# Kernel optimization log

Measured on AMD Instinct MI355X. Metric: run time of the kernel, lower is better.

## Reference

```python
import jax, jax.numpy as jnp
import numpy as np

B, S, D = 16, 1024, 1024
H = 8
QK = D // 8            # qk_dim = dim / qk_dim_div(8) = 128
EXP = D * 2            # expand_dim = dim * expand_factor(2) = 2048
V = D                  # v_dim = dim
RESIDUAL_DEPTH = 384   # hyp['net']['residual_depth'] (init scale only)
NUM_BLOCKS = 8         # hyp['net']['num_blocks'] (init scale only)
NEG = -1e30            # stand-in for -inf in the masked positions


def setup_inputs() -> dict:
    key = jax.random.key(0)
    k0, k1, k2 = jax.random.split(key, 3)
    x = jax.random.normal(k0, (B, S, D), jnp.float32)
    norm_w = jnp.ones((D,), jnp.float32)  # LayerNorm weight (bias=False)
    expand_w = (0.5 / RESIDUAL_DEPTH**0.5 / 2.0) * jax.random.normal(
        k1, (2 * QK + 2 * EXP, D), jnp.float32)
    project_w = (1.0 / RESIDUAL_DEPTH**0.5 / 2.0 / NUM_BLOCKS) * jax.random.normal(
        k2, (D, EXP), jnp.float32)
    pos_bias_mult = jnp.array(1.0, jnp.float32)
    return {
        "x": x,
        "norm_w": norm_w,
        "expand_w": expand_w,
        "project_w": project_w,
        "pos_bias_mult": pos_bias_mult,
        "first_acting_token_idx": 512,
        "last_acting_token_idx": 768,
    }


def _make_mask(pos_bias_mult, seq_len, first_idx, last_idx, dtype):
    idx = jnp.arange(seq_len)
    rel = (idx[None, :] - idx[:, None]).astype(dtype)   # j - i  (ALiBi-like)
    causal = idx[None, :] <= idx[:, None]               # tril incl. diagonal
    bias = jax.nn.softplus(pos_bias_mult) * rel
    mask = jnp.where(causal, bias, NEG)
    if first_idx is not None:
        assert last_idx is not None and last_idx > first_idx
        # torch: idx >= seq_len -> None -> slice from 0
        fi = 0 if first_idx >= seq_len else first_idx
        li = 0 if last_idx >= seq_len else last_idx
        override = (idx[:, None] >= fi) & (idx[None, :] >= li)
        mask = jnp.where(override, bias, mask)
    return mask


def reference(x, norm_w, expand_w, project_w, pos_bias_mult,
              first_acting_token_idx, last_acting_token_idx):
    Bx, Sx, Dx = x.shape
    residual = x
    mask = _make_mask(pos_bias_mult, Sx, first_acting_token_idx,
                      last_acting_token_idx, x.dtype)  # [S, S]

    # LayerNorm (bias-free)
    mu = x.mean(-1, keepdims=True)
    xc = x - mu
    var = (xc * xc).mean(-1, keepdims=True)
    xn = xc * jax.lax.rsqrt(var + 1e-5) * norm_w

    # fused expand projection, then split q / k / linear / pre_gelu
    proj = jnp.einsum('bsd,ed->bse', xn, expand_w)
    q = proj[..., :QK]
    k = proj[..., QK:2 * QK]
    lin = proj[..., 2 * QK:2 * QK + EXP]
    pre = proj[..., 2 * QK + EXP:]
    geglu = lin * jax.nn.gelu(pre, approximate=False)

    # linear_value = False: both local and attention-value come from geglu
    geglu_local = geglu[..., :EXP - V]   # [B, S, EXP-V]
    geglu_value = geglu[..., EXP - V:]   # [B, S, V]

    dh_q = QK // H
    dh_v = V // H
    qh = q.reshape(Bx, Sx, H, dh_q).transpose(0, 2, 1, 3)
    kh = k.reshape(Bx, Sx, H, dh_q).transpose(0, 2, 1, 3)
    vh = geglu_value.reshape(Bx, Sx, H, dh_v).transpose(0, 2, 1, 3)

    scale = 1.0 / np.sqrt(dh_q)  # SDPA default: 1/sqrt(E), E = query head dim
    scores = jnp.einsum('bhqd,bhkd->bhqk', qh, kh) * scale + mask
    attn = jax.nn.softmax(scores, axis=-1)
    outh = jnp.einsum('bhqk,bhkd->bhqd', attn, vh)
    attention = outh.transpose(0, 2, 1, 3).reshape(Bx, Sx, V)
    # NOTE: geglu_local's head rearrange + inverse rearrange is an identity.

    out = jnp.einsum('bse,de->bsd',
                     jnp.concatenate([geglu_local, attention], axis=-1),
                     project_w)
    return residual + out
```

## Files before the change

### kernel.cpp

```cpp
#include <hip/hip_runtime.h>
#include <hip/hip_bf16.h>
#include <cstdint>
#include <cstddef>

#define S_LEN   1024
#define D_DIM   1024
#define QK_DIM  128
#define EXP_DIM 2048
#define H_HEADS 8
#define DH_Q    16
#define DH_V    128
#define M_ROWS  16384

typedef __bf16 bf16;
typedef __bf16 b16x4 __attribute__((ext_vector_type(4)));
typedef __bf16 b16x8 __attribute__((ext_vector_type(8)));
typedef float  fx4   __attribute__((ext_vector_type(4)));
typedef float  f32x16 __attribute__((ext_vector_type(16)));

__device__ __forceinline__ void load_lds16(const bf16* g, bf16* l) {
    __builtin_amdgcn_global_load_lds(
        (const __attribute__((address_space(1))) void*)g,
        (__attribute__((address_space(3))) void*)l, 16, 0, 0);
}

__global__ __launch_bounds__(256) void convert_kernel(const float* __restrict__ src,
                                                      bf16* __restrict__ dst, int n4) {
    const int i = blockIdx.x * 256 + threadIdx.x;
    if (i >= n4) return;
    const fx4 v = ((const fx4*)src)[i];
    b16x4 o;
#pragma unroll
    for (int k = 0; k < 4; ++k) o[k] = (bf16)v[k];
    ((b16x4*)dst)[i] = o;
}

__global__ __launch_bounds__(256) void convert_expand_kernel(const float* __restrict__ src,
                                                             bf16* __restrict__ dst) {
    const int i = blockIdx.x * 256 + threadIdx.x;
    const int orow = i >> 8, col = i & 255;
    int irow;
    if (orow < 256) {
        irow = orow;
    } else {
        const int t = orow - 256;
        const int c = t >> 5, j = t & 31;
        irow = (j < 16) ? (256 + c * 16 + j) : (2304 + c * 16 + (j - 16));
    }
    const fx4 v = ((const fx4*)src)[irow * 256 + col];
    b16x4 o;
#pragma unroll
    for (int k = 0; k < 4; ++k) o[k] = (bf16)v[k];
    ((b16x4*)dst)[i] = o;
}

__global__ __launch_bounds__(256) void ln_kernel(const float* __restrict__ x,
                                                 const float* __restrict__ w,
                                                 bf16* __restrict__ xn) {
    const int row = blockIdx.x;
    const int tid = threadIdx.x;
    const fx4 t = ((const fx4*)x)[(size_t)row * 256 + tid];
    float v[4];
    float s = 0.f, ss = 0.f;
#pragma unroll
    for (int i = 0; i < 4; ++i) { v[i] = t[i]; s += v[i]; ss += v[i] * v[i]; }
#pragma unroll
    for (int off = 32; off >= 1; off >>= 1) {
        s  += __shfl_xor(s,  off);
        ss += __shfl_xor(ss, off);
    }
    __shared__ float ls[4], lss[4];
    const int wave = tid >> 6;
    if ((tid & 63) == 0) { ls[wave] = s; lss[wave] = ss; }
    __syncthreads();
    s  = ls[0]  + ls[1]  + ls[2]  + ls[3];
    ss = lss[0] + lss[1] + lss[2] + lss[3];
    const float mu  = s * (1.f / D_DIM);
    const float var = ss * (1.f / D_DIM) - mu * mu;
    const float r   = rsqrtf(var + 1e-5f);
    const fx4 w4 = ((const fx4*)w)[tid];
    b16x4 o4;
#pragma unroll
    for (int i = 0; i < 4; ++i) o4[i] = (bf16)((v[i] - mu) * r * w4[i]);
    ((b16x4*)(xn + (size_t)row * D_DIM))[tid] = o4;
}

__device__ __forceinline__ float gelu_exact(float x) {
    return 0.5f * x * (1.f + erff(x * 0.70710678118654752f));
}

__device__ __forceinline__ void tile_map(int& tm, int& tn) {
    const int NT = gridDim.x, MT = gridDim.y;
    const int lin = blockIdx.y * NT + blockIdx.x;
    if ((MT & 31) == 0 && (NT & 3) == 0) {
        const int xcd = lin & 7, slot = lin >> 3;
        const int MB  = MT >> 3;
        const int cnc = NT >> 2;
        const int c = slot >> 4, w = slot & 15;
        const int cm = c / cnc, cn = c - cm * cnc;
        tm = xcd * MB + cm * 4 + (w >> 2);
        tn = cn * 4 + (w & 3);
    } else { tm = blockIdx.y; tn = blockIdx.x; }
}

template <int EPI>
__global__ __launch_bounds__(256) void gemm_bt(const bf16* __restrict__ A,
                                               const bf16* __restrict__ W,
                                               const float* __restrict__ R,
                                               bf16* __restrict__ C,
                                               bf16* __restrict__ VH,
                                               float* __restrict__ OutF,
                                               int M, int N, int K) {
    __shared__ bf16 As[128 * 32];
    __shared__ bf16 Ws[128 * 32];
    const int tid  = threadIdx.x;
    const int wave = tid >> 6, lane = tid & 63;
    int tmi, tni;
    tile_map(tmi, tni);
    const int tile_n = tni * 128;
    const int tile_m = tmi * 128;
    const int m_off = (wave >> 1) * 64, n_off = (wave & 1) * 64;

    fx4 acc[4][4] = {};

    const int c0 = wave * 128 + lane;
    const int c1 = c0 + 64;
    const int r0 = c0 >> 2, cc0 = (c0 & 3) * 8;
    const int r1 = c1 >> 2, cc1 = (c1 & 3) * 8;

    const int mrow = lane & 15, quad = lane >> 4;

    for (int k0 = 0; k0 < K; k0 += 32) {
        load_lds16(A + (size_t)(tile_m + r0) * K + k0 + cc0, &As[c0 * 8]);
        load_lds16(A + (size_t)(tile_m + r1) * K + k0 + cc1, &As[c1 * 8]);
        load_lds16(W + (size_t)(tile_n + r0) * K + k0 + cc0, &Ws[c0 * 8]);
        load_lds16(W + (size_t)(tile_n + r1) * K + k0 + cc1, &Ws[c1 * 8]);
        __syncthreads();

        b16x8 af[4], bfr[4];
#pragma unroll
        for (int i = 0; i < 4; ++i) {
            af[i]  = *(const b16x8*)&As[(m_off + i * 16 + mrow) * 32 + quad * 8];
            bfr[i] = *(const b16x8*)&Ws[(n_off + i * 16 + mrow) * 32 + quad * 8];
        }
#pragma unroll
        for (int mi = 0; mi < 4; ++mi)
#pragma unroll
            for (int ni = 0; ni < 4; ++ni)
                acc[mi][ni] = __builtin_amdgcn_mfma_f32_16x16x32_bf16(
                    af[mi], bfr[ni], acc[mi][ni], 0, 0, 0);
        __syncthreads();
    }

    const int lcol = lane & 15, lrow4 = (lane >> 4) * 4;
    if (EPI == 2) {
        const int gbase = ((tile_n + n_off) >> 1) + lcol;
#pragma unroll
        for (int mi = 0; mi < 4; ++mi)
#pragma unroll
            for (int np = 0; np < 2; ++np) {
                const int gcol = gbase + np * 16;
#pragma unroll
                for (int r = 0; r < 4; ++r) {
                    const int gr = tile_m + m_off + mi * 16 + lrow4 + r;
                    const float l = acc[mi][2 * np][r];
                    const float p = acc[mi][2 * np + 1][r];
                    const float g = l * gelu_exact(p);
                    if (gcol < 1024) C[(size_t)gr * 2048 + gcol] = (bf16)g;
                    else             VH[(size_t)gr * 1024 + (gcol - 1024)] = (bf16)g;
                }
            }
    } else {
#pragma unroll
        for (int mi = 0; mi < 4; ++mi)
#pragma unroll
            for (int ni = 0; ni < 4; ++ni)
#pragma unroll
                for (int r = 0; r < 4; ++r) {
                    const int gr = tile_m + m_off + mi * 16 + lrow4 + r;
                    const int gc = tile_n + n_off + ni * 16 + lcol;
                    const float a = acc[mi][ni][r];
                    if (EPI == 0) {
                        C[(size_t)gr * N + gc] = (bf16)a;
                    } else {
                        const size_t idx = (size_t)gr * N + gc;
                        OutF[idx] = a + R[idx];
                    }
                }
    }
}

__global__ __launch_bounds__(512) void attn_kernel(const bf16* __restrict__ qk,
                                                   const bf16* __restrict__ vh,
                                                   const float* __restrict__ pbmv,
                                                   const int* __restrict__ fip,
                                                   const int* __restrict__ lip,
                                                   bf16* __restrict__ concatb) {
    const int lin = blockIdx.y * gridDim.x + blockIdx.x;
    const int xcd = lin & 7, slot = lin >> 3;
    const int bh = xcd * 16 + (slot >> 3);
    const int qt = slot & 7;
    const int b = bh >> 3, h = bh & 7;
    const int q0 = qt * 128;
    const int tid  = threadIdx.x;
    const int wave = tid >> 6, lane = tid & 63;
    const int lm = lane & 31, lh = lane >> 5;
    const int qq = wave >> 1, sect = wave & 1;

    __shared__ float Ps[128][68];
    __shared__ bf16  Pb[128][72];
    __shared__ bf16  Vt[128][72];
    __shared__ float Mrow[128], Lrow[128], Arow[128];

    const float pm = pbmv[0];
    const float sp = (pm > 20.f) ? pm : log1pf(expf(pm));
    int fi = fip[0], li = lip[0];
    if (fi >= S_LEN) fi = 0;
    if (li >= S_LEN) li = 0;

    const b16x8 qfrag = *(const b16x8*)(qk
        + ((size_t)(b * S_LEN + q0 + qq * 32 + lm)) * 256 + h * DH_Q + lh * 8);

    f32x16 accO[2] = {};
    if (tid < 128) { Mrow[tid] = -3e38f; Lrow[tid] = 0.f; }

    const int vkey = tid & 63;
    const int vd   = (tid >> 6) * 16;
    const int srow = wave * 16 + (lane >> 2);
    const int skq  = (lane & 3) * 16;

    const int qmax = q0 + 127;
    for (int k0 = 0; k0 < S_LEN; k0 += 64) {
        const bool any = (k0 <= qmax) || ((qmax >= fi) && (k0 + 63 >= li));
        if (!any) continue;

        __syncthreads();

#pragma unroll
        for (int i = 0; i < 2; ++i) {
            const int d0 = vd + i * 8;
            const b16x8 v8 = *(const b16x8*)(vh
                + ((size_t)(b * S_LEN + k0 + vkey)) * D_DIM + h * DH_V + d0);
#pragma unroll
            for (int j = 0; j < 8; ++j) Vt[d0 + j][vkey] = v8[j];
        }

        {
            const b16x8 kfrag = *(const b16x8*)(qk
                + ((size_t)(b * S_LEN + k0 + sect * 32 + lm)) * 256
                + QK_DIM + h * DH_Q + lh * 8);
            f32x16 z = {};
            const f32x16 S = __builtin_amdgcn_mfma_f32_32x32x16_bf16(qfrag, kfrag, z, 0, 0, 0);
#pragma unroll
            for (int r = 0; r < 16; ++r) {
                const int row = qq * 32 + (r & 3) + 8 * (r >> 2) + 4 * lh;
                Ps[row][sect * 32 + lm] = S[r];
            }
        }
        __syncthreads();

        {
            const int rg = q0 + srow;
            float s[16];
#pragma unroll
            for (int i = 0; i < 4; ++i) {
                const fx4 t = *(const fx4*)&Ps[srow][skq + i * 4];
#pragma unroll
                for (int j = 0; j < 4; ++j) {
                    const int jg = k0 + skq + i * 4 + j;
                    const bool act = (jg <= rg) || ((rg >= fi) && (jg >= li));
                    s[i * 4 + j] = act ? (t[j] * 0.25f + sp * (float)(jg - rg)) : -3e38f;
                }
            }
            float mloc = -3e38f;
#pragma unroll
            for (int i = 0; i < 16; ++i) mloc = fmaxf(mloc, s[i]);
            mloc = fmaxf(mloc, __shfl_xor(mloc, 1));
            mloc = fmaxf(mloc, __shfl_xor(mloc, 2));
            const float m_old = Mrow[srow];
            const float m_new = fmaxf(m_old, mloc);
            const float alpha = (m_old <= -1e29f) ? 0.f : expf(m_old - m_new);
            float lsum = 0.f;
            b16x8 p0, p1;
#pragma unroll
            for (int i = 0; i < 16; ++i) {
                const float p = (s[i] <= -1e29f) ? 0.f : expf(s[i] - m_new);
                lsum += p;
                if (i < 8) p0[i] = (bf16)p; else p1[i - 8] = (bf16)p;
            }
            lsum += __shfl_xor(lsum, 1);
            lsum += __shfl_xor(lsum, 2);
            *(b16x8*)&Pb[srow][skq]     = p0;
            *(b16x8*)&Pb[srow][skq + 8] = p1;
            if ((lane & 3) == 0) {
                Mrow[srow] = m_new;
                Lrow[srow] = alpha * Lrow[srow] + lsum;
                Arow[srow] = alpha;
            }
        }
        __syncthreads();

        {
#pragma unroll
            for (int r = 0; r < 16; ++r) {
                const float al = Arow[qq * 32 + (r & 3) + 8 * (r >> 2) + 4 * lh];
                accO[0][r] *= al;
                accO[1][r] *= al;
            }
            b16x8 Af[4];
#pragma unroll
            for (int ks = 0; ks < 4; ++ks)
                Af[ks] = *(const b16x8*)&Pb[qq * 32 + lm][ks * 16 + lh * 8];
#pragma unroll
            for (int nb = 0; nb < 2; ++nb)
#pragma unroll
                for (int ks = 0; ks < 4; ++ks) {
                    const b16x8 Bf = *(const b16x8*)&Vt[sect * 64 + nb * 32 + lm][ks * 16 + lh * 8];
                    accO[nb] = __builtin_amdgcn_mfma_f32_32x32x16_bf16(Af[ks], Bf, accO[nb], 0, 0, 0);
                }
        }
    }

#pragma unroll
    for (int r = 0; r < 16; ++r) {
        const int row = qq * 32 + (r & 3) + 8 * (r >> 2) + 4 * lh;
        const float L = Lrow[row];
        const float inv = (L > 0.f) ? 1.f / L : 0.f;
        const size_t base = ((size_t)(b * S_LEN + q0 + row)) * EXP_DIM
                          + EXP_DIM / 2 + h * DH_V + sect * 64 + lm;
#pragma unroll
        for (int nb = 0; nb < 2; ++nb)
            concatb[base + nb * 32] = (bf16)(accO[nb][r] * inv);
    }
}

static constexpr size_t WS0_OFF = 0;
static constexpr size_t QK_OFF  = 67108864;
static constexpr size_t VH_OFF  = QK_OFF + 8388608;
static constexpr size_t EW_OFF  = VH_OFF + 33554432;
static constexpr size_t PW_OFF  = EW_OFF + 8912896;
static constexpr size_t WS_NEED = PW_OFF + 4194304;

extern "C" void kernel_launch(void* const* d_in, const int* in_sizes, int n_in,
                              void* d_out, int out_size, void* d_ws, size_t ws_size,
                              hipStream_t stream) {
    const float* x         = (const float*)d_in[0];
    const float* norm_w    = (const float*)d_in[1];
    const float* expand_w  = (const float*)d_in[2];
    const float* project_w = (const float*)d_in[3];
    const float* pbm       = (const float*)d_in[4];
    const int*   fip       = (const int*)d_in[5];
    const int*   lip       = (const int*)d_in[6];
    float* out = (float*)d_out;

    if (ws_size < WS_NEED) return;

    char* ws = (char*)d_ws;
    bf16* ws0 = (bf16*)(ws + WS0_OFF);
    bf16* qkb = (bf16*)(ws + QK_OFF);
    bf16* vh  = (bf16*)(ws + VH_OFF);
    bf16* ewb = (bf16*)(ws + EW_OFF);
    bf16* pwb = (bf16*)(ws + PW_OFF);
    bf16* xn  = (bf16*)d_out;

    convert_expand_kernel<<<4352, 256, 0, stream>>>(expand_w, ewb);
    convert_kernel<<<2048, 256, 0, stream>>>(project_w, pwb, 2097152 / 4);
    ln_kernel<<<M_ROWS, 256, 0, stream>>>(x, norm_w, xn);

    gemm_bt<0><<<dim3(2, M_ROWS / 128), 256, 0, stream>>>(
        xn, ewb, nullptr, qkb, nullptr, nullptr, M_ROWS, 256, D_DIM);
    gemm_bt<2><<<dim3(32, M_ROWS / 128), 256, 0, stream>>>(
        xn, ewb + (size_t)256 * D_DIM, nullptr, ws0, vh, nullptr, M_ROWS, 4096, D_DIM);
    attn_kernel<<<dim3(64, 16), 512, 0, stream>>>(qkb, vh, pbm, fip, lip, ws0);
    gemm_bt<1><<<dim3(8, M_ROWS / 128), 256, 0, stream>>>(
        ws0, pwb, x, nullptr, nullptr, out, M_ROWS, D_DIM, EXP_DIM);
}
```

Before: 605.6 us.

## Add 256x256-tile GEMM kernel with swizzled LDS and interleaved prefetch

Adds a new gemm256 kernel using 256x256 output tiles, 512 threads, BK=64 double-buffered LDS loaded via direct global-to-LDS transfers with an XOR swizzle to reduce bank conflicts. Loads for the next k-tile are interleaved with four MFMA phases, separated by barriers and raised wave priority. The large GEGLU expand GEMM and the output projection GEMM now use this kernel. The aim is higher arithmetic intensity and better overlap of memory with compute, at the cost of more registers and LDS per block and therefore lower occupancy.

```diff
diff --git a/kernel.cpp b/kernel.cpp
--- a/kernel.cpp
+++ b/kernel.cpp
@@ -90,6 +90,20 @@
 }
 
 __device__ __forceinline__ void tile_map(int& tm, int& tn) {
+    const int NT = gridDim.x, MT = gridDim.y;
+    const int lin = blockIdx.y * NT + blockIdx.x;
+    if ((MT & 31) == 0 && (NT & 3) == 0) {
+        const int xcd = lin & 7, slot = lin >> 3;
+        const int MB  = MT >> 3;
+        const int cnc = NT >> 2;
+        const int c = slot >> 4, w = slot & 15;
+        const int cm = c / cnc, cn = c - cm * cnc;
+        tm = xcd * MB + cm * 4 + (w >> 2);
+        tn = cn * 4 + (w & 3);
+    } else { tm = blockIdx.y; tn = blockIdx.x; }
+}
+
+__device__ __forceinline__ void tile_map256(int& tm, int& tn) {
     const int NT = gridDim.x, MT = gridDim.y;
     const int lin = blockIdx.y * NT + blockIdx.x;
     if ((MT & 31) == 0 && (NT & 3) == 0) {
@@ -153,16 +167,187 @@
     }
 
     const int lcol = lane & 15, lrow4 = (lane >> 4) * 4;
+#pragma unroll
+    for (int mi = 0; mi < 4; ++mi)
+#pragma unroll
+        for (int ni = 0; ni < 4; ++ni)
+#pragma unroll
+            for (int r = 0; r < 4; ++r) {
+                const int gr = tile_m + m_off + mi * 16 + lrow4 + r;
+                const int gc = tile_n + n_off + ni * 16 + lcol;
+                const float a = acc[mi][ni][r];
+                if (EPI == 0) {
+                    C[(size_t)gr * N + gc] = (bf16)a;
+                } else if (EPI == 1) {
+                    const size_t idx = (size_t)gr * N + gc;
+                    OutF[idx] = a + R[idx];
+                }
+            }
+}
+
+__device__ __forceinline__ b16x8 lds_frag_swz(const bf16* buf, int r, int c) {
+    const int q = r * 128 + c * 2;
+    const int p = q ^ (((q >> 9) & 1) << 5);
+    return *(const b16x8*)((const char*)buf + p);
+}
+
+template <int EPI>
+__global__ __launch_bounds__(512, 2) void gemm256(const bf16* __restrict__ A,
+                                                  const bf16* __restrict__ W,
+                                                  const float* __restrict__ R,
+                                                  bf16* __restrict__ C,
+                                                  bf16* __restrict__ VH,
+                                                  float* __restrict__ OutF,
+                                                  int M, int N, int K) {
+    __shared__ bf16 Abuf[2][16384];
+    __shared__ bf16 Bbuf[2][16384];
+    const int tid  = threadIdx.x;
+    const int wave = tid >> 6, lane = tid & 63;
+    const int wm = wave >> 2, wn = wave & 3;
+    const int l15 = lane & 15, quad = lane >> 4;
+
+    int tmi, tni;
+    tile_map256(tmi, tni);
+    const int tile_m = tmi * 256, tile_n = tni * 256;
+
+    size_t offA[4], offB[4];
+#pragma unroll
+    for (int s = 0; s < 4; ++s) {
+        const int d = s * 8192 + tid * 16;
+        const int q = d ^ (((d >> 9) & 1) << 5);
+        const int r = q >> 7, c = (q >> 1) & 63;
+        offA[s] = (size_t)(tile_m + r) * K + c;
+        offB[s] = (size_t)(tile_n + r) * K + c;
+    }
+    const int ldst = tid * 16;
+
+    fx4 acc[8][4] = {};
+
+    const int ntk = K >> 6;
+#pragma unroll
+    for (int s = 0; s < 4; ++s) {
+        load_lds16(A + offA[s], (bf16*)((char*)&Abuf[0][0] + s * 8192 + ldst));
+        load_lds16(W + offB[s], (bf16*)((char*)&Bbuf[0][0] + s * 8192 + ldst));
+    }
+
+    for (int t = 0; t < ntk; ++t) {
+        const int nb = t & 1;
+        __syncthreads();
+        const int kt1 = (t + 1) << 6;
+        const bool pf = (t + 1 < ntk);
+        const bf16* ab = &Abuf[nb][0];
+        const bf16* bb = &Bbuf[nb][0];
+        char* adst = (char*)&Abuf[nb ^ 1][0] + ldst;
+        char* bdst = (char*)&Bbuf[nb ^ 1][0] + ldst;
+
+        b16x8 af[4][2];
+        b16x8 bfv[2][2];
+
+        if (pf) {
+            load_lds16(A + offA[0] + kt1, (bf16*)(adst));
+            load_lds16(A + offA[1] + kt1, (bf16*)(adst + 8192));
+        }
+#pragma unroll
+        for (int mi = 0; mi < 4; ++mi)
+#pragma unroll
+            for (int kk = 0; kk < 2; ++kk)
+                af[mi][kk] = lds_frag_swz(ab, wm * 128 + mi * 16 + l15, kk * 32 + quad * 8);
+#pragma unroll
+        for (int ni = 0; ni < 2; ++ni)
+#pragma unroll
+            for (int kk = 0; kk < 2; ++kk)
+                bfv[ni][kk] = lds_frag_swz(bb, wn * 64 + ni * 16 + l15, kk * 32 + quad * 8);
+        __builtin_amdgcn_s_barrier();
+        __builtin_amdgcn_s_setprio(1);
+#pragma unroll
+        for (int mi = 0; mi < 4; ++mi)
+#pragma unroll
+            for (int ni = 0; ni < 2; ++ni)
+#pragma unroll
+                for (int kk = 0; kk < 2; ++kk)
+                    acc[mi][ni] = __builtin_amdgcn_mfma_f32_16x16x32_bf16(
+                        af[mi][kk], bfv[ni][kk], acc[mi][ni], 0, 0, 0);
+        __builtin_amdgcn_s_setprio(0);
+        __builtin_amdgcn_s_barrier();
+
+        if (pf) {
+            load_lds16(A + offA[2] + kt1, (bf16*)(adst + 16384));
+            load_lds16(A + offA[3] + kt1, (bf16*)(adst + 24576));
+        }
+#pragma unroll
+        for (int ni = 0; ni < 2; ++ni)
+#pragma unroll
+            for (int kk = 0; kk < 2; ++kk)
+                bfv[ni][kk] = lds_frag_swz(bb, wn * 64 + (ni + 2) * 16 + l15, kk * 32 + quad * 8);
+        __builtin_amdgcn_s_barrier();
+        __builtin_amdgcn_s_setprio(1);
+#pragma unroll
+        for (int mi = 0; mi < 4; ++mi)
+#pragma unroll
+            for (int ni = 0; ni < 2; ++ni)
+#pragma unroll
+                for (int kk = 0; kk < 2; ++kk)
+                    acc[mi][ni + 2] = __builtin_amdgcn_mfma_f32_16x16x32_bf16(
+                        af[mi][kk], bfv[ni][kk], acc[mi][ni + 2], 0, 0, 0);
+        __builtin_amdgcn_s_setprio(0);
+        __builtin_amdgcn_s_barrier();
+
+        if (pf) {
+            load_lds16(W + offB[0] + kt1, (bf16*)(bdst));
+            load_lds16(W + offB[1] + kt1, (bf16*)(bdst + 8192));
+        }
+#pragma unroll
+        for (int mi = 0; mi < 4; ++mi)
+#pragma unroll
+            for (int kk = 0; kk < 2; ++kk)
+                af[mi][kk] = lds_frag_swz(ab, wm * 128 + (mi + 4) * 16 + l15, kk * 32 + quad * 8);
+        __builtin_amdgcn_s_barrier();
+        __builtin_amdgcn_s_setprio(1);
+#pragma unroll
+        for (int mi = 0; mi < 4; ++mi)
+#pragma unroll
+            for (int ni = 0; ni < 2; ++ni)
+#pragma unroll
+                for (int kk = 0; kk < 2; ++kk)
+                    acc[mi + 4][ni + 2] = __builtin_amdgcn_mfma_f32_16x16x32_bf16(
+                        af[mi][kk], bfv[ni][kk], acc[mi + 4][ni + 2], 0, 0, 0);
+        __builtin_amdgcn_s_setprio(0);
+        __builtin_amdgcn_s_barrier();
+
+        if (pf) {
+            load_lds16(W + offB[2] + kt1, (bf16*)(bdst + 16384));
+            load_lds16(W + offB[3] + kt1, (bf16*)(bdst + 24576));
+        }
+#pragma unroll
+        for (int ni = 0; ni < 2; ++ni)
+#pragma unroll
+            for (int kk = 0; kk < 2; ++kk)
+                bfv[ni][kk] = lds_frag_swz(bb, wn * 64 + ni * 16 + l15, kk * 32 + quad * 8);
+        __builtin_amdgcn_s_barrier();
+        __builtin_amdgcn_s_setprio(1);
+#pragma unroll
+        for (int mi = 0; mi < 4; ++mi)
+#pragma unroll
+            for (int ni = 0; ni < 2; ++ni)
+#pragma unroll
+                for (int kk = 0; kk < 2; ++kk)
+                    acc[mi + 4][ni] = __builtin_amdgcn_mfma_f32_16x16x32_bf16(
+                        af[mi][kk], bfv[ni][kk], acc[mi + 4][ni], 0, 0, 0);
+        __builtin_amdgcn_s_setprio(0);
+        __builtin_amdgcn_s_barrier();
+    }
+
+    const int rbase = tile_m + wm * 128 + quad * 4;
     if (EPI == 2) {
-        const int gbase = ((tile_n + n_off) >> 1) + lcol;
-#pragma unroll
-        for (int mi = 0; mi < 4; ++mi)
+        const int gb = ((tile_n + wn * 64) >> 1) + l15;
+#pragma unroll
+        for (int mi = 0; mi < 8; ++mi)
 #pragma unroll
             for (int np = 0; np < 2; ++np) {
-                const int gcol = gbase + np * 16;
+                const int gcol = gb + np * 16;
 #pragma unroll
                 for (int r = 0; r < 4; ++r) {
-                    const int gr = tile_m + m_off + mi * 16 + lrow4 + r;
+                    const int gr = rbase + mi * 16 + r;
                     const float l = acc[mi][2 * np][r];
                     const float p = acc[mi][2 * np + 1][r];
                     const float g = l * gelu_exact(p);
@@ -172,13 +357,13 @@
             }
     } else {
 #pragma unroll
-        for (int mi = 0; mi < 4; ++mi)
+        for (int mi = 0; mi < 8; ++mi)
 #pragma unroll
             for (int ni = 0; ni < 4; ++ni)
 #pragma unroll
                 for (int r = 0; r < 4; ++r) {
-                    const int gr = tile_m + m_off + mi * 16 + lrow4 + r;
-                    const int gc = tile_n + n_off + ni * 16 + lcol;
+                    const int gr = rbase + mi * 16 + r;
+                    const int gc = tile_n + wn * 64 + ni * 16 + l15;
                     const float a = acc[mi][ni][r];
                     if (EPI == 0) {
                         C[(size_t)gr * N + gc] = (bf16)a;
@@ -369,9 +554,9 @@
 
     gemm_bt<0><<<dim3(2, M_ROWS / 128), 256, 0, stream>>>(
         xn, ewb, nullptr, qkb, nullptr, nullptr, M_ROWS, 256, D_DIM);
-    gemm_bt<2><<<dim3(32, M_ROWS / 128), 256, 0, stream>>>(
+    gemm256<2><<<dim3(16, M_ROWS / 256), 512, 0, stream>>>(
         xn, ewb + (size_t)256 * D_DIM, nullptr, ws0, vh, nullptr, M_ROWS, 4096, D_DIM);
     attn_kernel<<<dim3(64, 16), 512, 0, stream>>>(qkb, vh, pbm, fip, lip, ws0);
-    gemm_bt<1><<<dim3(8, M_ROWS / 128), 256, 0, stream>>>(
+    gemm256<1><<<dim3(4, M_ROWS / 256), 512, 0, stream>>>(
         ws0, pwb, x, nullptr, nullptr, out, M_ROWS, D_DIM, EXP_DIM);
 }
```

After: 628.0 us. +3.7%, slower.
